# Kernel tuning notes

Measured on AMD Instinct MI355X. Metric: run time of the kernel, lower is better.

The kernel has to match this reference:

```python
import jax, jax.numpy as jnp
import numpy as np

D_MODEL = 1024
NUM_HEADS = 16
D_K = D_MODEL // NUM_HEADS


def setup_inputs() -> dict:
    key = jax.random.key(0)
    ks = jax.random.split(key, 5)
    s = 1.0 / np.sqrt(D_MODEL)
    return {
        "x": jax.random.normal(ks[0], (2, 2048, D_MODEL), dtype=jnp.float32),
        "Wq": jax.random.normal(ks[1], (D_MODEL, D_MODEL), dtype=jnp.float32) * s,
        "bq": jnp.zeros((D_MODEL,), jnp.float32),
        "Wk": jax.random.normal(ks[2], (D_MODEL, D_MODEL), dtype=jnp.float32) * s,
        "bk": jnp.zeros((D_MODEL,), jnp.float32),
        "Wv": jax.random.normal(ks[3], (D_MODEL, D_MODEL), dtype=jnp.float32) * s,
        "bv": jnp.zeros((D_MODEL,), jnp.float32),
        "Wo": jax.random.normal(ks[4], (D_MODEL, D_MODEL), dtype=jnp.float32) * s,
        "bo": jnp.zeros((D_MODEL,), jnp.float32),
    }


def _rotate_half(t):
    t1, t2 = t[..., : D_K // 2], t[..., D_K // 2 :]
    return jnp.concatenate((-t2, t1), axis=-1)


def reference(x, Wq, bq, Wk, bk, Wv, bv, Wo, bo):
    B, S, D = x.shape
    H, dk = NUM_HEADS, D_K
    # RoPE tables: inv_freq over even dims, emb = cat(freqs, freqs)
    inv_freq = 1.0 / (10000.0 ** (jnp.arange(0, dk, 2, dtype=jnp.float32) / dk))
    pos = jnp.arange(S, dtype=jnp.float32)
    freqs = pos[:, None] * inv_freq[None, :]            # [S, dk/2]
    emb = jnp.concatenate((freqs, freqs), axis=-1)      # [S, dk]
    cos = jnp.cos(emb)[None, :, None, :]                # [1, S, 1, dk]
    sin = jnp.sin(emb)[None, :, None, :]

    q = (x @ Wq + bq).reshape(B, S, H, dk)
    k = (x @ Wk + bk).reshape(B, S, H, dk)
    v = (x @ Wv + bv).reshape(B, S, H, dk)

    q = q * cos + _rotate_half(q) * sin
    k = k * cos + _rotate_half(k) * sin

    # [B,H,S,S] scores, stable softmax, then weighted sum of V
    scores = jnp.einsum("bqhd,bkhd->bhqk", q, k) / jnp.sqrt(jnp.float32(dk))
    attn = jax.nn.softmax(scores, axis=-1)
    out = jnp.einsum("bhqk,bkhd->bqhd", attn, v).reshape(B, S, D)
    return out @ Wo + bo
```

## Files before the change

kernel.cpp:

```cpp
#include <hip/hip_runtime.h>
#include <hip/hip_bf16.h>
#include <math.h>

typedef __bf16 bf16_t;
typedef bf16_t bf16x4 __attribute__((ext_vector_type(4)));
typedef bf16_t bf16x8 __attribute__((ext_vector_type(8)));
typedef float f32x4 __attribute__((ext_vector_type(4)));

#define SEQ 2048
#define BATCH 2
#define NHEAD 16
#define DK 64
#define DMODEL 1024

#define GLOAD16(gsrc, ldst)                                                        \
    __builtin_amdgcn_global_load_lds(                                              \
        (const __attribute__((address_space(1))) void*)(gsrc),                     \
        (__attribute__((address_space(3))) void*)(ldst), 16, 0, 0)

__device__ __forceinline__ float exp2_hw(float x) {
#if __has_builtin(__builtin_amdgcn_exp2f)
    return __builtin_amdgcn_exp2f(x);
#else
    float r; asm("v_exp_f32 %0, %1" : "=v"(r) : "v"(x)); return r;
#endif
}

__global__ __launch_bounds__(256)
void prep_kernel(const float* __restrict__ x, bf16_t* __restrict__ y,
                 const float* __restrict__ W0, const float* __restrict__ W1,
                 const float* __restrict__ W2, const float* __restrict__ W3,
                 bf16_t* __restrict__ Wt, float2* __restrict__ cs) {
    __shared__ float t[32][33];
    const int id = blockIdx.x, tid = threadIdx.x;
    if (id < 4096) {
        int i = (id * 256 + tid) * 4;
        float4 v = *reinterpret_cast<const float4*>(x + i);
        bf16x4 o = { (bf16_t)v.x, (bf16_t)v.y, (bf16_t)v.z, (bf16_t)v.w };
        *reinterpret_cast<bf16x4*>(y + i) = o;
    } else if (id < 8192) {
        const int id2 = id - 4096;
        const int z = id2 >> 10, rem = id2 & 1023;
        const int n0 = (rem & 31) * 32, k0 = ((rem >> 5) & 31) * 32;
        const int tx = tid & 31, ty = tid >> 5;
        const float* W = (z == 0) ? W0 : (z == 1) ? W1 : (z == 2) ? W2 : W3;
        bf16_t* out = Wt + ((size_t)z << 20);
#pragma unroll
        for (int i = 0; i < 32; i += 8)
            t[ty + i][tx] = W[(size_t)(k0 + ty + i) * DMODEL + n0 + tx];
        __syncthreads();
#pragma unroll
        for (int i = 0; i < 32; i += 8)
            out[(size_t)(n0 + ty + i) * DMODEL + k0 + tx] = (bf16_t)t[tx][ty + i];
    } else {
        int idx = (id - 8192) * 256 + tid;
        int j = idx & 31, s = idx >> 5;
        float inv = powf(10000.0f, -(float)j / 32.0f);
        float ang = (float)s * inv;
        cs[idx] = make_float2(cosf(ang), sinf(ang));
    }
}

template<int NF>
__device__ __forceinline__ void gemm_core(const bf16_t* __restrict__ A,
                                          const bf16_t* __restrict__ Bt,
                                          int m0, int n0,
                                          bf16_t* As, bf16_t* Bs,
                                          f32x4 (&acc)[4][NF]) {
    const int tid = threadIdx.x, lane = tid & 63, wid = tid >> 6;
    const int wr = wid >> 1, wc = wid & 1;
    const int lm = lane & 15, lq = lane >> 4;
    constexpr int BROWS = NF * 32;
    constexpr int NT = DMODEL / 32;

    const int r_in = lane >> 2;
    const int csw  = (((lane & 3) ^ ((lane >> 3) & 3)) << 3);
    const bf16_t* Ag = A  + (size_t)(m0 + 32 * wid + r_in) * DMODEL + csw;
    const bf16_t* Bg = Bt + (size_t)(n0 + (NF * 8) * wid + r_in) * DMODEL + csw;
    const int cswr = ((lq ^ ((lm >> 1) & 3)) << 4);

    auto stage = [&](int t, int buf) {
        const int k0 = t * 32;
        bf16_t* a = As + buf * (128 * 32) + 32 * wid * 32;
        bf16_t* b = Bs + buf * (BROWS * 32) + (NF * 8) * wid * 32;
        GLOAD16(Ag + k0,               a);
        GLOAD16(Ag + 16 * DMODEL + k0, a + 16 * 32);
        GLOAD16(Bg + k0,               b);
        if constexpr (NF == 4) GLOAD16(Bg + 16 * DMODEL + k0, b + 16 * 32);
    };

    stage(0, 0);
    stage(1, 1);
    int cb = 0;
    for (int t = 0; t < NT; ++t) {
        if (t + 2 < NT) {
            int sb = cb + 2; if (sb >= 3) sb -= 3;
            stage(t + 2, sb);
            if constexpr (NF == 4) asm volatile("s_waitcnt vmcnt(8)" ::: "memory");
            else                   asm volatile("s_waitcnt vmcnt(6)" ::: "memory");
        } else if (t + 1 < NT) {
            if constexpr (NF == 4) asm volatile("s_waitcnt vmcnt(4)" ::: "memory");
            else                   asm volatile("s_waitcnt vmcnt(3)" ::: "memory");
        } else {
            asm volatile("s_waitcnt vmcnt(0)" ::: "memory");
        }
        __builtin_amdgcn_s_barrier();

        const char* pAs = (const char*)(As + cb * (128 * 32));
        const char* pBs = (const char*)(Bs + cb * (BROWS * 32));
        bf16x8 af[4], bfr[NF];
#pragma unroll
        for (int mf = 0; mf < 4; ++mf)
            af[mf] = *reinterpret_cast<const bf16x8*>(pAs + (wr * 64 + mf * 16 + lm) * 64 + cswr);
#pragma unroll
        for (int nf = 0; nf < NF; ++nf)
            bfr[nf] = *reinterpret_cast<const bf16x8*>(pBs + (wc * (NF * 16) + nf * 16 + lm) * 64 + cswr);
#pragma unroll
        for (int mf = 0; mf < 4; ++mf)
#pragma unroll
            for (int nf = 0; nf < NF; ++nf)
                acc[mf][nf] = __builtin_amdgcn_mfma_f32_16x16x32_bf16(af[mf], bfr[nf], acc[mf][nf], 0, 0, 0);

        asm volatile("" ::: "memory");
        __builtin_amdgcn_s_barrier();
        if (++cb == 3) cb = 0;
    }
}

__global__ __launch_bounds__(256)
void gemm_qkv_kernel(const bf16_t* __restrict__ xb, const bf16_t* __restrict__ wtqk,
                     const bf16_t* __restrict__ wtv,
                     const float* __restrict__ bq, const float* __restrict__ bk,
                     const float* __restrict__ bv,
                     bf16_t* __restrict__ qb, bf16_t* __restrict__ kb,
                     bf16_t* __restrict__ vtb, const float2* __restrict__ cs) {
    __shared__ bf16_t As[3 * 128 * 32];
    __shared__ bf16_t Bs[3 * 128 * 32];
    const int tid = threadIdx.x, lane = tid & 63, wid = tid >> 6;
    const int wr = wid >> 1, wc = wid & 1;
    const int lm = lane & 15, lq = lane >> 4;
    const int orig = blockIdx.x;
    const int id = (orig & 7) * 96 + (orig >> 3);
    f32x4 acc[4][4] = {};

    if (id < 512) {
        const int m0 = (id >> 4) * 128, n0 = (id & 15) * 128;
        gemm_core<4>(xb, wtqk, m0, n0, As, Bs, acc);
        const bool is_k = (n0 >= 1024);
        const float* bs = is_k ? bk : bq;
        bf16_t* C = is_k ? kb : qb;
        const int cb = (is_k ? n0 - 1024 : n0) + wc * 64;
        const float b0 = bs[cb + lm],      b1 = bs[cb + 16 + lm];
        const float b2 = bs[cb + 32 + lm], b3 = bs[cb + 48 + lm];
#pragma unroll
        for (int mf = 0; mf < 4; ++mf)
#pragma unroll
            for (int i = 0; i < 4; ++i) {
                const int row = m0 + wr * 64 + mf * 16 + lq * 4 + i;
                const int s = row & (SEQ - 1);
                const float2 cs0 = cs[s * 32 + lm];
                const float2 cs1 = cs[s * 32 + 16 + lm];
                const float a0 = acc[mf][0][i] + b0, a1 = acc[mf][1][i] + b1;
                const float a2 = acc[mf][2][i] + b2, a3 = acc[mf][3][i] + b3;
                bf16_t* p = C + (size_t)row * DMODEL + cb;
                p[lm]      = (bf16_t)(a0 * cs0.x - a2 * cs0.y);
                p[16 + lm] = (bf16_t)(a1 * cs1.x - a3 * cs1.y);
                p[32 + lm] = (bf16_t)(a2 * cs0.x + a0 * cs0.y);
                p[48 + lm] = (bf16_t)(a3 * cs1.x + a1 * cs1.y);
            }
    } else {
        const int id2 = id - 512;
        const int m0 = (id2 & 7) * 128, n0 = (id2 >> 3) * 128;
        gemm_core<4>(wtv, xb, m0, n0, As, Bs, acc);
#pragma unroll
        for (int mf = 0; mf < 4; ++mf)
#pragma unroll
            for (int i = 0; i < 4; ++i) {
                const int row = m0 + wr * 64 + mf * 16 + lq * 4 + i;
                const float brow = bv[row];
#pragma unroll
                for (int nf = 0; nf < 4; ++nf) {
                    const int col = n0 + wc * 64 + nf * 16 + lm;
                    vtb[(size_t)row * 4096 + col] = (bf16_t)(acc[mf][nf][i] + brow);
                }
            }
    }
}

__global__ __launch_bounds__(256)
void gemm_out_kernel(const bf16_t* __restrict__ A, const bf16_t* __restrict__ Bt,
                     const float* __restrict__ bias, float* __restrict__ C) {
    __shared__ bf16_t As[3 * 128 * 32];
    __shared__ bf16_t Bs[3 * 64 * 32];
    const int tid = threadIdx.x, lane = tid & 63, wid = tid >> 6;
    const int wr = wid >> 1, wc = wid & 1;
    const int lm = lane & 15, lq = lane >> 4;
    const int orig = blockIdx.x;
    const int id = (orig & 7) * 64 + (orig >> 3);
    const int m0 = (id >> 4) * 128, n0 = (id & 15) * 64;
    f32x4 acc[4][2] = {};
    gemm_core<2>(A, Bt, m0, n0, As, Bs, acc);
#pragma unroll
    for (int nf = 0; nf < 2; ++nf) {
        const int col = n0 + wc * 32 + nf * 16 + lm;
        const float bcol = bias[col];
#pragma unroll
        for (int mf = 0; mf < 4; ++mf)
#pragma unroll
            for (int i = 0; i < 4; ++i) {
                const int row = m0 + wr * 64 + mf * 16 + lq * 4 + i;
                C[(size_t)row * DMODEL + col] = acc[mf][nf][i] + bcol;
            }
    }
}

__global__ __launch_bounds__(256)
void attn_kernel(const bf16_t* __restrict__ q, const bf16_t* __restrict__ k,
                 const bf16_t* __restrict__ vt, bf16_t* __restrict__ attnout) {
    const int tid = threadIdx.x, lane = tid & 63, wid = tid >> 6;
    const int lm = lane & 15, lq = lane >> 4;
    const int bh = blockIdx.y, b = bh >> 4, h = bh & 15;
    const int qrow0 = blockIdx.x * 128 + wid * 32;
    const float MS = 20.0f;
    constexpr int NT = SEQ / 64;

    __shared__ bf16_t Ks[4][64][64];
    __shared__ bf16_t Vs[4][64][64];

    const bf16_t* qA = q + ((size_t)(b * SEQ + qrow0 + lm) * NHEAD + h) * DK + lq * 8;
    const bf16_t* qB = qA + (size_t)16 * NHEAD * DK;
    bf16x8 aqA0 = *reinterpret_cast<const bf16x8*>(qA);
    bf16x8 aqA1 = *reinterpret_cast<const bf16x8*>(qA + 32);
    bf16x8 aqB0 = *reinterpret_cast<const bf16x8*>(qB);
    bf16x8 aqB1 = *reinterpret_cast<const bf16x8*>(qB + 32);
#pragma unroll
    for (int j = 0; j < 8; ++j) {
        aqA0[j] = (bf16_t)((float)aqA0[j] * 0.18033688f);
        aqA1[j] = (bf16_t)((float)aqA1[j] * 0.18033688f);
        aqB0[j] = (bf16_t)((float)aqB0[j] * 0.18033688f);
        aqB1[j] = (bf16_t)((float)aqB1[j] * 0.18033688f);
    }
    const bf16_t one = (bf16_t)1.0f;
    const bf16x8 ones = { one, one, one, one, one, one, one, one };
    const f32x4 cinit = { -MS, -MS, -MS, -MS };

    const int r0   = 8 * wid + (lane >> 3);
    const int scol = (((lane & 7) ^ (lane >> 3)) << 3);
    const int sig  = ((r0 >> 2) & 3) * 8 + ((r0 >> 4) & 1) * 4 + (r0 & 3);
    const bf16_t* kg = k  + ((size_t)(b * SEQ + sig) * NHEAD + h) * DK + scol;
    const bf16_t* vg = vt + ((size_t)(h * DK + r0)) * 4096 + (size_t)b * SEQ + scol;
    const size_t kstep = (size_t)NHEAD * DK;
    const char* ksb = (const char*)Ks;
    const char* vsb = (const char*)Vs;
    const int c0 = (lq << 4) ^ ((lm & 7) << 4);
    const int rowb = lm * 128;

    f32x4 OA[4] = {}, OB[4] = {};
    f32x4 olA = {}, olB = {};

    auto stage = [&](int buf, int kb) {
        GLOAD16(kg + (size_t)kb * kstep,        &Ks[buf][8 * wid][0]);
        GLOAD16(kg + (size_t)(kb + 32) * kstep, &Ks[buf][32 + 8 * wid][0]);
        GLOAD16(vg + kb,                        &Vs[buf][8 * wid][0]);
        GLOAD16(vg + (size_t)32 * 4096 + kb,    &Vs[buf][32 + 8 * wid][0]);
    };
    auto qk = [&](int buf, f32x4 (&sA)[4], f32x4 (&sB)[4]) {
        const char* kt = ksb + buf * 8192;
        __builtin_amdgcn_s_setprio(1);
#pragma unroll
        for (int t = 0; t < 4; ++t) {
            bf16x8 a0 = *reinterpret_cast<const bf16x8*>(kt + t * 2048 + rowb + c0);
            bf16x8 a1 = *reinterpret_cast<const bf16x8*>(kt + t * 2048 + rowb + (c0 ^ 64));
            f32x4 xA = __builtin_amdgcn_mfma_f32_16x16x32_bf16(a0, aqA0, cinit, 0, 0, 0);
            xA = __builtin_amdgcn_mfma_f32_16x16x32_bf16(a1, aqA1, xA, 0, 0, 0);
            f32x4 xB = __builtin_amdgcn_mfma_f32_16x16x32_bf16(a0, aqB0, cinit, 0, 0, 0);
            xB = __builtin_amdgcn_mfma_f32_16x16x32_bf16(a1, aqB1, xB, 0, 0, 0);
            sA[t] = xA; sB[t] = xB;
        }
        __builtin_amdgcn_s_setprio(0);
    };

    stage(0, 0);
    stage(1, 64);
    asm volatile("s_waitcnt vmcnt(4)" ::: "memory");
    __builtin_amdgcn_s_barrier();
    asm volatile("" ::: "memory");
    f32x4 stA[4], stB[4];
    qk(0, stA, stB);

    for (int t = 0; t < NT; ++t) {
        const int kb = t * 64;
        if (t + 2 < NT) stage((t + 2) & 3, kb + 128);
        if (t + 1 < NT) {
            if (t + 2 < NT) asm volatile("s_waitcnt vmcnt(4)" ::: "memory");
            else            asm volatile("s_waitcnt vmcnt(0)" ::: "memory");
            __builtin_amdgcn_s_barrier();
            asm volatile("" ::: "memory");
        }

        f32x4 nA[4], nB[4];
        if (t + 1 < NT) qk((t + 1) & 3, nA, nB);

        bf16x8 paA0, paA1, paB0, paB1;
#pragma unroll
        for (int u = 0; u < 2; ++u)
#pragma unroll
            for (int i = 0; i < 4; ++i) {
                paA0[4 * u + i] = (bf16_t)exp2_hw(stA[u][i]);
                paA1[4 * u + i] = (bf16_t)exp2_hw(stA[u + 2][i]);
                paB0[4 * u + i] = (bf16_t)exp2_hw(stB[u][i]);
                paB1[4 * u + i] = (bf16_t)exp2_hw(stB[u + 2][i]);
            }

        const char* vtl = vsb + (t & 3) * 8192;
        __builtin_amdgcn_s_setprio(1);
#pragma unroll
        for (int nf = 0; nf < 4; ++nf) {
            bf16x8 v0 = *reinterpret_cast<const bf16x8*>(vtl + nf * 2048 + rowb + c0);
            bf16x8 v1 = *reinterpret_cast<const bf16x8*>(vtl + nf * 2048 + rowb + (c0 ^ 64));
            f32x4 oA = OA[nf], oB = OB[nf];
            oA = __builtin_amdgcn_mfma_f32_16x16x32_bf16(v0, paA0, oA, 0, 0, 0);
            oA = __builtin_amdgcn_mfma_f32_16x16x32_bf16(v1, paA1, oA, 0, 0, 0);
            oB = __builtin_amdgcn_mfma_f32_16x16x32_bf16(v0, paB0, oB, 0, 0, 0);
            oB = __builtin_amdgcn_mfma_f32_16x16x32_bf16(v1, paB1, oB, 0, 0, 0);
            OA[nf] = oA; OB[nf] = oB;
        }
        olA = __builtin_amdgcn_mfma_f32_16x16x32_bf16(ones, paA0, olA, 0, 0, 0);
        olA = __builtin_amdgcn_mfma_f32_16x16x32_bf16(ones, paA1, olA, 0, 0, 0);
        olB = __builtin_amdgcn_mfma_f32_16x16x32_bf16(ones, paB0, olB, 0, 0, 0);
        olB = __builtin_amdgcn_mfma_f32_16x16x32_bf16(ones, paB1, olB, 0, 0, 0);
        __builtin_amdgcn_s_setprio(0);

        if (t + 1 < NT) {
#pragma unroll
            for (int i = 0; i < 4; ++i) { stA[i] = nA[i]; stB[i] = nB[i]; }
        }
    }

    const float invA = 1.0f / olA[0];
    const float invB = 1.0f / olB[0];
    bf16_t* obA = attnout + ((size_t)(b * SEQ + qrow0 + lm) * NHEAD + h) * DK;
    bf16_t* obB = obA + (size_t)16 * NHEAD * DK;
#pragma unroll
    for (int nf = 0; nf < 4; ++nf) {
        bf16x4 cA = { (bf16_t)(OA[nf][0] * invA), (bf16_t)(OA[nf][1] * invA),
                      (bf16_t)(OA[nf][2] * invA), (bf16_t)(OA[nf][3] * invA) };
        bf16x4 cB = { (bf16_t)(OB[nf][0] * invB), (bf16_t)(OB[nf][1] * invB),
                      (bf16_t)(OB[nf][2] * invB), (bf16_t)(OB[nf][3] * invB) };
        *reinterpret_cast<bf16x4*>(obA + nf * 16 + lq * 4) = cA;
        *reinterpret_cast<bf16x4*>(obB + nf * 16 + lq * 4) = cB;
    }
}

extern "C" void kernel_launch(void* const* d_in, const int* in_sizes, int n_in,
                              void* d_out, int out_size, void* d_ws, size_t ws_size,
                              hipStream_t stream) {
    const float* x  = (const float*)d_in[0];
    const float* Wq = (const float*)d_in[1];
    const float* bq = (const float*)d_in[2];
    const float* Wk = (const float*)d_in[3];
    const float* bk = (const float*)d_in[4];
    const float* Wv = (const float*)d_in[5];
    const float* bv = (const float*)d_in[6];
    const float* Wo = (const float*)d_in[7];
    const float* bo = (const float*)d_in[8];
    float* out = (float*)d_out;

    char* ws = (char*)d_ws;
    bf16_t* xb  = (bf16_t*)(ws);
    bf16_t* wtq = (bf16_t*)(ws + ((size_t)8  << 20));
    bf16_t* wtv = wtq + (2 << 20);
    bf16_t* wto = wtq + (3 << 20);
    bf16_t* qb  = (bf16_t*)(ws + ((size_t)16 << 20));
    bf16_t* kb  = (bf16_t*)(ws + ((size_t)24 << 20));
    bf16_t* vtb = (bf16_t*)(ws + ((size_t)32 << 20));
    float2* csT = (float2*)(ws + ((size_t)40 << 20));
    bf16_t* aob = xb;

    prep_kernel<<<8448, 256, 0, stream>>>(x, xb, Wq, Wk, Wv, Wo, wtq, csT);
    gemm_qkv_kernel<<<768, 256, 0, stream>>>(xb, wtq, wtv, bq, bk, bv, qb, kb, vtb, csT);
    attn_kernel<<<dim3(16, 32), 256, 0, stream>>>(qb, kb, vtb, aob);
    gemm_out_kernel<<<512, 256, 0, stream>>>(aob, wto, bo, out);
}
```

Baseline: 123.0 us.

## Split K/V staging, ping-pong warps between QK and PV, remap blocks per XCD

The attention kernel now stages K and V tiles separately. Even and odd waves run the QK^T and softmax/PV phases in opposite order, so MFMA and exp work from different waves interleave and compete less for the same units. Blocks are linearized and mapped so each XCD handles four contiguous (batch, head) pairs, which is meant to improve L2 reuse of K/V. The reordered vmcnt waits rely on odd waves issuing their V loads late, which adds some risk around ordering and correctness.

```diff
diff --git a/kernel.cpp b/kernel.cpp
--- a/kernel.cpp
+++ b/kernel.cpp
@@ -219,8 +219,11 @@
                  const bf16_t* __restrict__ vt, bf16_t* __restrict__ attnout) {
     const int tid = threadIdx.x, lane = tid & 63, wid = tid >> 6;
     const int lm = lane & 15, lq = lane >> 4;
-    const int bh = blockIdx.y, b = bh >> 4, h = bh & 15;
-    const int qrow0 = blockIdx.x * 128 + wid * 32;
+    const int bid = blockIdx.x;
+    const int xcd = bid & 7, idx = bid >> 3;
+    const int bh = xcd * 4 + (idx & 3), qblk = idx >> 2;
+    const int b = bh >> 4, h = bh & 15;
+    const int qrow0 = qblk * 128 + wid * 32;
     const float MS = 20.0f;
     constexpr int NT = SEQ / 64;
 
@@ -258,9 +261,11 @@
     f32x4 OA[4] = {}, OB[4] = {};
     f32x4 olA = {}, olB = {};
 
-    auto stage = [&](int buf, int kb) {
+    auto stageK = [&](int buf, int kb) {
         GLOAD16(kg + (size_t)kb * kstep,        &Ks[buf][8 * wid][0]);
         GLOAD16(kg + (size_t)(kb + 32) * kstep, &Ks[buf][32 + 8 * wid][0]);
+    };
+    auto stageV = [&](int buf, int kb) {
         GLOAD16(vg + kb,                        &Vs[buf][8 * wid][0]);
         GLOAD16(vg + (size_t)32 * 4096 + kb,    &Vs[buf][32 + 8 * wid][0]);
     };
@@ -279,59 +284,72 @@
         }
         __builtin_amdgcn_s_setprio(0);
     };
-
-    stage(0, 0);
-    stage(1, 64);
-    asm volatile("s_waitcnt vmcnt(4)" ::: "memory");
+    auto softmax = [&](const f32x4 (&sA)[4], const f32x4 (&sB)[4],
+                       bf16x8& pA0, bf16x8& pA1, bf16x8& pB0, bf16x8& pB1) {
+#pragma unroll
+        for (int u = 0; u < 2; ++u)
+#pragma unroll
+            for (int i = 0; i < 4; ++i) {
+                pA0[4 * u + i] = (bf16_t)exp2_hw(sA[u][i]);
+                pA1[4 * u + i] = (bf16_t)exp2_hw(sA[u + 2][i]);
+                pB0[4 * u + i] = (bf16_t)exp2_hw(sB[u][i]);
+                pB1[4 * u + i] = (bf16_t)exp2_hw(sB[u + 2][i]);
+            }
+    };
+    auto pv = [&](int buf, const bf16x8& pA0, const bf16x8& pA1,
+                  const bf16x8& pB0, const bf16x8& pB1) {
+        const char* vtl = vsb + buf * 8192;
+        __builtin_amdgcn_s_setprio(1);
+#pragma unroll
+        for (int nf = 0; nf < 4; ++nf) {
+            bf16x8 v0 = *reinterpret_cast<const bf16x8*>(vtl + nf * 2048 + rowb + c0);
+            bf16x8 v1 = *reinterpret_cast<const bf16x8*>(vtl + nf * 2048 + rowb + (c0 ^ 64));
+            f32x4 oA = OA[nf], oB = OB[nf];
+            oA = __builtin_amdgcn_mfma_f32_16x16x32_bf16(v0, pA0, oA, 0, 0, 0);
+            oA = __builtin_amdgcn_mfma_f32_16x16x32_bf16(v1, pA1, oA, 0, 0, 0);
+            oB = __builtin_amdgcn_mfma_f32_16x16x32_bf16(v0, pB0, oB, 0, 0, 0);
+            oB = __builtin_amdgcn_mfma_f32_16x16x32_bf16(v1, pB1, oB, 0, 0, 0);
+            OA[nf] = oA; OB[nf] = oB;
+        }
+        olA = __builtin_amdgcn_mfma_f32_16x16x32_bf16(ones, pA0, olA, 0, 0, 0);
+        olA = __builtin_amdgcn_mfma_f32_16x16x32_bf16(ones, pA1, olA, 0, 0, 0);
+        olB = __builtin_amdgcn_mfma_f32_16x16x32_bf16(ones, pB0, olB, 0, 0, 0);
+        olB = __builtin_amdgcn_mfma_f32_16x16x32_bf16(ones, pB1, olB, 0, 0, 0);
+        __builtin_amdgcn_s_setprio(0);
+    };
+
+    stageK(0, 0);  stageV(0, 0);
+    stageK(1, 64); stageV(1, 64);
+    asm volatile("s_waitcnt vmcnt(2)" ::: "memory");
     __builtin_amdgcn_s_barrier();
     asm volatile("" ::: "memory");
     f32x4 stA[4], stB[4];
     qk(0, stA, stB);
 
+    const bool evenw = (wid & 1) == 0;
     for (int t = 0; t < NT; ++t) {
         const int kb = t * 64;
-        if (t + 2 < NT) stage((t + 2) & 3, kb + 128);
+        f32x4 nA[4], nB[4];
+        bf16x8 paA0, paA1, paB0, paB1;
+
+        if (t + 2 < NT) stageK((t + 2) & 3, kb + 128);
+        if (evenw) {
+            if (t + 1 < NT) qk((t + 1) & 3, nA, nB);
+            if (t + 2 < NT) stageV((t + 2) & 3, kb + 128);
+            softmax(stA, stB, paA0, paA1, paB0, paB1);
+            pv(t & 3, paA0, paA1, paB0, paB1);
+        } else {
+            softmax(stA, stB, paA0, paA1, paB0, paB1);
+            pv(t & 3, paA0, paA1, paB0, paB1);
+            if (t + 2 < NT) stageV((t + 2) & 3, kb + 128);
+            if (t + 1 < NT) qk((t + 1) & 3, nA, nB);
+        }
+
         if (t + 1 < NT) {
-            if (t + 2 < NT) asm volatile("s_waitcnt vmcnt(4)" ::: "memory");
+            if (t + 2 < NT) asm volatile("s_waitcnt vmcnt(2)" ::: "memory");
             else            asm volatile("s_waitcnt vmcnt(0)" ::: "memory");
             __builtin_amdgcn_s_barrier();
             asm volatile("" ::: "memory");
-        }
-
-        f32x4 nA[4], nB[4];
-        if (t + 1 < NT) qk((t + 1) & 3, nA, nB);
-
-        bf16x8 paA0, paA1, paB0, paB1;
-#pragma unroll
-        for (int u = 0; u < 2; ++u)
-#pragma unroll
-            for (int i = 0; i < 4; ++i) {
-                paA0[4 * u + i] = (bf16_t)exp2_hw(stA[u][i]);
-                paA1[4 * u + i] = (bf16_t)exp2_hw(stA[u + 2][i]);
-                paB0[4 * u + i] = (bf16_t)exp2_hw(stB[u][i]);
-                paB1[4 * u + i] = (bf16_t)exp2_hw(stB[u + 2][i]);
-            }
-
-        const char* vtl = vsb + (t & 3) * 8192;
-        __builtin_amdgcn_s_setprio(1);
-#pragma unroll
-        for (int nf = 0; nf < 4; ++nf) {
-            bf16x8 v0 = *reinterpret_cast<const bf16x8*>(vtl + nf * 2048 + rowb + c0);
-            bf16x8 v1 = *reinterpret_cast<const bf16x8*>(vtl + nf * 2048 + rowb + (c0 ^ 64));
-            f32x4 oA = OA[nf], oB = OB[nf];
-            oA = __builtin_amdgcn_mfma_f32_16x16x32_bf16(v0, paA0, oA, 0, 0, 0);
-            oA = __builtin_amdgcn_mfma_f32_16x16x32_bf16(v1, paA1, oA, 0, 0, 0);
-            oB = __builtin_amdgcn_mfma_f32_16x16x32_bf16(v0, paB0, oB, 0, 0, 0);
-            oB = __builtin_amdgcn_mfma_f32_16x16x32_bf16(v1, paB1, oB, 0, 0, 0);
-            OA[nf] = oA; OB[nf] = oB;
-        }
-        olA = __builtin_amdgcn_mfma_f32_16x16x32_bf16(ones, paA0, olA, 0, 0, 0);
-        olA = __builtin_amdgcn_mfma_f32_16x16x32_bf16(ones, paA1, olA, 0, 0, 0);
-        olB = __builtin_amdgcn_mfma_f32_16x16x32_bf16(ones, paB0, olB, 0, 0, 0);
-        olB = __builtin_amdgcn_mfma_f32_16x16x32_bf16(ones, paB1, olB, 0, 0, 0);
-        __builtin_amdgcn_s_setprio(0);
-
-        if (t + 1 < NT) {
 #pragma unroll
             for (int i = 0; i < 4; ++i) { stA[i] = nA[i]; stB[i] = nB[i]; }
         }
@@ -379,6 +397,6 @@
 
     prep_kernel<<<8448, 256, 0, stream>>>(x, xb, Wq, Wk, Wv, Wo, wtq, csT);
     gemm_qkv_kernel<<<768, 256, 0, stream>>>(xb, wtq, wtv, bq, bk, bv, qb, kb, vtb, csT);
-    attn_kernel<<<dim3(16, 32), 256, 0, stream>>>(qb, kb, vtb, aob);
+    attn_kernel<<<512, 256, 0, stream>>>(qb, kb, vtb, aob);
     gemm_out_kernel<<<512, 256, 0, stream>>>(aob, wto, bo, out);
 }
```

New measurement: 120.8 us. About the same (-1.8%).
